# Performance work log

Measured on AMD Instinct MI355X. Metric: run time of the kernel, lower is better.

The kernel has to match this reference:

```python
import jax, jax.numpy as jnp
import numpy as np

B, Q, T, H, W = 8, 100, 50, 256, 256
COST_MASK_W = 1.0  # init kwarg cost_mask
COST_DICE_W = 1.0  # init kwarg cost_dice


def setup_inputs() -> dict:
    key = jax.random.key(0)
    k1, k2 = jax.random.split(key)
    pred_masks = jax.random.normal(k1, (B, Q, H, W), dtype=jnp.float32)
    # binary GT masks (0/1), already at prediction resolution so nearest-interp is identity
    tgt_masks = jax.random.randint(k2, (B, T, H, W), 0, 2).astype(jnp.int32)
    return {"pred_masks": pred_masks, "tgt_masks": tgt_masks}


def reference(pred_masks, tgt_masks):
    # pred_masks: [B, Q, H, W] logits; tgt_masks: [B, T, H, W] binary
    b, q = pred_masks.shape[:2]
    x = pred_masks.reshape(b, q, -1)                      # [B, Q, HW]
    t = tgt_masks.reshape(b, tgt_masks.shape[1], -1).astype(x.dtype)  # [B, T, HW]
    hw = x.shape[-1]

    # batch_sigmoid_ce_loss: BCE-with-logits vs all-ones / all-zeros targets
    pos = jax.nn.softplus(-x)                             # BCE(x, 1)
    neg = jax.nn.softplus(x)                              # BCE(x, 0)
    cost_ce = (jnp.einsum('bqc,btc->bqt', pos, t)
               + jnp.einsum('bqc,btc->bqt', neg, 1.0 - t)) / hw

    # batch_dice_loss
    s = jax.nn.sigmoid(x)
    numerator = 2.0 * jnp.einsum('bqc,btc->bqt', s, t)
    denominator = s.sum(-1)[:, :, None] + t.sum(-1)[:, None, :]
    cost_dice = 1.0 - (numerator + 1.0) / (denominator + 1.0)

    # per-batch cost matrix C [B, Q, T]; the scipy Hungarian step is a
    # host-side CPU call outside the accelerator workload.
    return COST_MASK_W * cost_ce + COST_DICE_W * cost_dice
```

## Files before the change

### kernel.cpp

```cpp
#include <hip/hip_runtime.h>
#include <math.h>

#define B_ 8
#define Q_ 100
#define T_ 50
#define HW_ 65536

#define NSEG 64
#define SEG (HW_ / NSEG)
#define NK32 (SEG / 32)
#define NSTR 52

#define DSZ (B_ * Q_ * NSTR)
#define WS_D1 0
#define WS_D2 DSZ
#define WS_SNEG (2 * DSZ)
#define WS_ST (2 * DSZ + B_ * Q_)
#define WS_TOTAL (2 * DSZ + B_ * Q_ + B_ * T_)

#define PSEG 64
#define SEGP (HW_ / PSEG)
#define NK32P (SEGP / 32)
#define PROWS 101
#define PCOLS 52
#define PTILE ((size_t)PROWS * PCOLS)
#define PBLK ((size_t)B_ * PTILE)
#define D2OFF ((size_t)PSEG * PBLK)
#define WS_NEEDED_BYTES (2ull * D2OFF * 4ull)

typedef __attribute__((ext_vector_type(8))) short bf16x8;
typedef __attribute__((ext_vector_type(4))) float f32x4;

__device__ __forceinline__ unsigned short f2bf(float f) {
    union { float f; unsigned u; } v; v.f = f;
    unsigned r = v.u + 0x7FFF + ((v.u >> 16) & 1);
    return (unsigned short)(r >> 16);
}

__global__ __launch_bounds__(256, 2) void gemm_fused_p(const float* __restrict__ pred,
                                                       const int* __restrict__ tgt,
                                                       float* __restrict__ ws) {
    const int seg = blockIdx.x;
    const int b   = blockIdx.y;
    const int tid = threadIdx.x;
    const int wave = tid >> 6;
    const int lane = tid & 63;
    const int quad = lane >> 4;
    const int l16  = lane & 15;

    const float* xptr[2];
    int aones[2];
#pragma unroll
    for (int mt = 0; mt < 2; ++mt) {
        int m = (wave + mt * 4) * 16 + l16;
        aones[mt] = (m == Q_);
        int mr = m < Q_ ? m : Q_ - 1;
        xptr[mt] = pred + ((size_t)b * Q_ + mr) * HW_ + (size_t)seg * SEGP + quad * 8;
    }
    const int* tptr[4];
    short onesv[4];
#pragma unroll
    for (int nt = 0; nt < 4; ++nt) {
        int n = nt * 16 + l16;
        onesv[nt] = (n == T_) ? (short)0x3F80 : (short)0;
        int nr = n < T_ ? n : T_ - 1;
        tptr[nt] = tgt + ((size_t)b * T_ + nr) * HW_ + (size_t)seg * SEGP + quad * 8;
    }

    f32x4 accx[2][4], accs[2][4];
#pragma unroll
    for (int mt = 0; mt < 2; ++mt)
#pragma unroll
        for (int nt = 0; nt < 4; ++nt) {
            accx[mt][nt] = (f32x4)(0.f);
            accs[mt][nt] = (f32x4)(0.f);
        }
    float sneg[2] = {0.f, 0.f};

    float4 xrb[2][2][2];
    int4   trb[2][4][2];

    auto loadraw = [&](int ch, float4 xr[2][2], int4 tr[4][2]) {
        const int k = ch * 32;
#pragma unroll
        for (int mt = 0; mt < 2; ++mt) {
            xr[mt][0] = *(const float4*)(xptr[mt] + k);
            xr[mt][1] = *(const float4*)(xptr[mt] + k + 4);
        }
#pragma unroll
        for (int nt = 0; nt < 4; ++nt) {
            tr[nt][0] = *(const int4*)(tptr[nt] + k);
            tr[nt][1] = *(const int4*)(tptr[nt] + k + 4);
        }
    };

    auto compute = [&](float4 xr[2][2], int4 tr[4][2]) {
        bf16x8 tf[4];
#pragma unroll
        for (int nt = 0; nt < 4; ++nt)
#pragma unroll
            for (int h = 0; h < 2; ++h)
#pragma unroll
                for (int e = 0; e < 4; ++e) {
                    int v = (&tr[nt][h].x)[e];
                    tf[nt][h * 4 + e] = v ? (short)0x3F80 : onesv[nt];
                }
#pragma unroll
        for (int mt = 0; mt < 2; ++mt) {
            bf16x8 xf, sf;
            float sp = 0.f;
#pragma unroll
            for (int h = 0; h < 2; ++h)
#pragma unroll
                for (int e = 0; e < 4; ++e) {
                    float x = (&xr[mt][h].x)[e];
                    float ax = fabsf(x);
                    float ee = __expf(-ax);
                    float d = 1.f + ee;
                    float r1 = __builtin_amdgcn_rcpf(d);
                    float sg = (x >= 0.f) ? r1 : ee * r1;
                    sp += fmaxf(x, 0.f) + 0.69314718056f * __log2f(d);
                    xf[h * 4 + e] = aones[mt] ? (short)0x3F80 : (short)f2bf(x);
                    sf[h * 4 + e] = aones[mt] ? (short)0x3F80 : (short)f2bf(sg);
                }
            sneg[mt] += sp;
#pragma unroll
            for (int nt = 0; nt < 4; ++nt) {
                accx[mt][nt] = __builtin_amdgcn_mfma_f32_16x16x32_bf16(xf, tf[nt], accx[mt][nt], 0, 0, 0);
                accs[mt][nt] = __builtin_amdgcn_mfma_f32_16x16x32_bf16(sf, tf[nt], accs[mt][nt], 0, 0, 0);
            }
        }
    };

    loadraw(0, xrb[0], trb[0]);
#pragma unroll 2
    for (int ch = 0; ch < NK32P; ++ch) {
        const int cb = ch & 1;
        if (ch + 1 < NK32P) loadraw(ch + 1, xrb[cb ^ 1], trb[cb ^ 1]);
        compute(xrb[cb], trb[cb]);
    }

    float* d1 = ws + (size_t)(seg * B_ + b) * PTILE;
    float* d2 = d1 + D2OFF;

#pragma unroll
    for (int mt = 0; mt < 2; ++mt) {
        float v = sneg[mt];
        v += __shfl_xor(v, 16);
        v += __shfl_xor(v, 32);
        int m = (wave + mt * 4) * 16 + l16;
        if (quad == 0 && m < Q_) d1[(size_t)m * PCOLS + 51] = v;
    }
#pragma unroll
    for (int mt = 0; mt < 2; ++mt) {
        int mtile = (wave + mt * 4) * 16;
#pragma unroll
        for (int nt = 0; nt < 4; ++nt) {
            int n = nt * 16 + l16;
#pragma unroll
            for (int r = 0; r < 4; ++r) {
                int m = mtile + quad * 4 + r;
                if (m <= Q_ && n <= T_) {
                    size_t idx = (size_t)m * PCOLS + n;
                    d1[idx] = accx[mt][nt][r];
                    d2[idx] = accs[mt][nt][r];
                }
            }
        }
    }
}

__global__ void finalize_p(const float* __restrict__ ws, float* __restrict__ out) {
    int i = blockIdx.x * blockDim.x + threadIdx.x;
    if (i >= B_ * Q_ * T_) return;
    int b = i / (Q_ * T_);
    int r = i % (Q_ * T_);
    int q = r / T_;
    int t = r % T_;
    const float* d1 = ws;
    const float* d2 = ws + D2OFF;
    size_t offq = ((size_t)b * PROWS + q) * PCOLS;
    size_t offo = ((size_t)b * PROWS + Q_) * PCOLS;
    float dx = 0.f, ds = 0.f, ss = 0.f, sn = 0.f, stv = 0.f;
#pragma unroll 4
    for (int s = 0; s < PSEG; ++s) {
        size_t base = (size_t)s * PBLK + (size_t)b * PTILE;
        dx  += d1[base + (size_t)q * PCOLS + t];
        ds  += d2[base + (size_t)q * PCOLS + t];
        ss  += d2[base + (size_t)q * PCOLS + T_];
        sn  += d1[base + (size_t)q * PCOLS + 51];
        stv += d1[base + (size_t)Q_ * PCOLS + t];
    }
    (void)offq; (void)offo;
    float ce = (sn - dx) * (1.f / (float)HW_);
    float dice = 1.f - (2.f * ds + 1.f) / (ss + stv + 1.f);
    out[i] = ce + dice;
}

__global__ void zero_ws(float* ws) {
    int i = blockIdx.x * blockDim.x + threadIdx.x;
    if (i < WS_TOTAL) ws[i] = 0.f;
}

__global__ __launch_bounds__(256, 2) void gemm_fused(const float* __restrict__ pred,
                                                     const int* __restrict__ tgt,
                                                     float* __restrict__ ws) {
    const int seg = blockIdx.x;
    const int b   = blockIdx.y;
    const int tid = threadIdx.x;
    const int wave = tid >> 6;
    const int lane = tid & 63;
    const int quad = lane >> 4;
    const int l16  = lane & 15;

    const float* xptr[2];
#pragma unroll
    for (int mt = 0; mt < 2; ++mt) {
        int m = (wave + mt * 4) * 16 + l16;
        int mr = m < Q_ ? m : Q_ - 1;
        xptr[mt] = pred + ((size_t)b * Q_ + mr) * HW_ + (size_t)seg * SEG + quad * 8;
    }
    const int* tptr[4];
    int ones[4];
#pragma unroll
    for (int nt = 0; nt < 4; ++nt) {
        int n = nt * 16 + l16;
        ones[nt] = (n == T_);
        int nr = n < T_ ? n : T_ - 1;
        tptr[nt] = tgt + ((size_t)b * T_ + nr) * HW_ + (size_t)seg * SEG + quad * 8;
    }

    f32x4 accx[2][4], accs[2][4];
#pragma unroll
    for (int mt = 0; mt < 2; ++mt)
#pragma unroll
        for (int nt = 0; nt < 4; ++nt) {
            accx[mt][nt] = (f32x4)(0.f);
            accs[mt][nt] = (f32x4)(0.f);
        }
    float sneg[2] = {0.f, 0.f};
    float stq[4] = {0.f, 0.f, 0.f, 0.f};

    float4 xrb[2][2][2];
    int4   trb[2][4][2];

    auto loadraw = [&](int ch, float4 xr[2][2], int4 tr[4][2]) {
        const int k = ch * 32;
#pragma unroll
        for (int mt = 0; mt < 2; ++mt) {
            xr[mt][0] = *(const float4*)(xptr[mt] + k);
            xr[mt][1] = *(const float4*)(xptr[mt] + k + 4);
        }
#pragma unroll
        for (int nt = 0; nt < 4; ++nt) {
            tr[nt][0] = *(const int4*)(tptr[nt] + k);
            tr[nt][1] = *(const int4*)(tptr[nt] + k + 4);
        }
    };

    auto compute = [&](float4 xr[2][2], int4 tr[4][2]) {
        bf16x8 tf[4];
#pragma unroll
        for (int nt = 0; nt < 4; ++nt) {
            float cnt = 0.f;
#pragma unroll
            for (int h = 0; h < 2; ++h)
#pragma unroll
                for (int e = 0; e < 4; ++e) {
                    int v = (&tr[nt][h].x)[e];
                    tf[nt][h * 4 + e] = (v || ones[nt]) ? (short)0x3F80 : (short)0;
                    cnt += v ? 1.f : 0.f;
                }
            stq[nt] += cnt;
        }
#pragma unroll
        for (int mt = 0; mt < 2; ++mt) {
            bf16x8 xf, sf;
            float sp = 0.f;
#pragma unroll
            for (int h = 0; h < 2; ++h)
#pragma unroll
                for (int e = 0; e < 4; ++e) {
                    float x = (&xr[mt][h].x)[e];
                    float ax = fabsf(x);
                    float ee = __expf(-ax);
                    float d = 1.f + ee;
                    float r1 = __builtin_amdgcn_rcpf(d);
                    float sg = (x >= 0.f) ? r1 : ee * r1;
                    sp += fmaxf(x, 0.f) + 0.69314718056f * __log2f(d);
                    xf[h * 4 + e] = (short)f2bf(x);
                    sf[h * 4 + e] = (short)f2bf(sg);
                }
            sneg[mt] += sp;
#pragma unroll
            for (int nt = 0; nt < 4; ++nt) {
                accx[mt][nt] = __builtin_amdgcn_mfma_f32_16x16x32_bf16(xf, tf[nt], accx[mt][nt], 0, 0, 0);
                accs[mt][nt] = __builtin_amdgcn_mfma_f32_16x16x32_bf16(sf, tf[nt], accs[mt][nt], 0, 0, 0);
            }
        }
    };

    loadraw(0, xrb[0], trb[0]);
#pragma unroll 2
    for (int ch = 0; ch < NK32; ++ch) {
        const int cb = ch & 1;
        if (ch + 1 < NK32) loadraw(ch + 1, xrb[cb ^ 1], trb[cb ^ 1]);
        compute(xrb[cb], trb[cb]);
    }

#pragma unroll
    for (int mt = 0; mt < 2; ++mt) {
        float v = sneg[mt];
        v += __shfl_xor(v, 16);
        v += __shfl_xor(v, 32);
        int m = (wave + mt * 4) * 16 + l16;
        if (quad == 0 && m < Q_) atomicAdd(&ws[WS_SNEG + b * Q_ + m], v);
    }
    if (wave == 0) {
#pragma unroll
        for (int nt = 0; nt < 4; ++nt) {
            float v = stq[nt];
            v += __shfl_xor(v, 16);
            v += __shfl_xor(v, 32);
            int n = nt * 16 + l16;
            if (quad == 0 && n < T_) atomicAdd(&ws[WS_ST + b * T_ + n], v);
        }
    }
#pragma unroll
    for (int mt = 0; mt < 2; ++mt) {
        int mtile = (wave + mt * 4) * 16;
#pragma unroll
        for (int nt = 0; nt < 4; ++nt) {
            int n = nt * 16 + l16;
#pragma unroll
            for (int r = 0; r < 4; ++r) {
                int m = mtile + quad * 4 + r;
                if (m < Q_) {
                    size_t idx = ((size_t)b * Q_ + m) * NSTR + n;
                    if (n < T_) atomicAdd(&ws[WS_D1 + idx], accx[mt][nt][r]);
                    if (n <= T_) atomicAdd(&ws[WS_D2 + idx], accs[mt][nt][r]);
                }
            }
        }
    }
}

__global__ void finalize(const float* __restrict__ ws, float* __restrict__ out) {
    int i = blockIdx.x * blockDim.x + threadIdx.x;
    if (i >= B_ * Q_ * T_) return;
    int b = i / (Q_ * T_);
    int r = i % (Q_ * T_);
    int q = r / T_;
    int t = r % T_;
    float dx   = ws[WS_D1 + ((size_t)b * Q_ + q) * NSTR + t];
    float ds   = ws[WS_D2 + ((size_t)b * Q_ + q) * NSTR + t];
    float ssum = ws[WS_D2 + ((size_t)b * Q_ + q) * NSTR + T_];
    float st   = ws[WS_ST + b * T_ + t];
    float sneg = ws[WS_SNEG + b * Q_ + q];
    float ce = (sneg - dx) * (1.f / (float)HW_);
    float dice = 1.f - (2.f * ds + 1.f) / (ssum + st + 1.f);
    out[i] = ce + dice;
}

extern "C" void kernel_launch(void* const* d_in, const int* in_sizes, int n_in,
                              void* d_out, int out_size, void* d_ws, size_t ws_size,
                              hipStream_t stream) {
    const float* pred = (const float*)d_in[0];
    const int* tgt = (const int*)d_in[1];
    float* ws = (float*)d_ws;
    float* out = (float*)d_out;

    if (ws_size >= WS_NEEDED_BYTES) {
        dim3 g(PSEG, B_, 1);
        gemm_fused_p<<<g, 256, 0, stream>>>(pred, tgt, ws);
        finalize_p<<<(B_ * Q_ * T_ + 255) / 256, 256, 0, stream>>>(ws, out);
    } else {
        zero_ws<<<(WS_TOTAL + 255) / 256, 256, 0, stream>>>(ws);
        dim3 g(NSEG, B_, 1);
        gemm_fused<<<g, 256, 0, stream>>>(pred, tgt, ws);
        finalize<<<(B_ * Q_ * T_ + 255) / 256, 256, 0, stream>>>(ws, out);
    }
}
```

Before: 382.3 us.

## Bit-pack target masks and split-K GEMM with two-stage partial reduction

Adds a pre-pass that uses wave ballots to pack the int32 target masks into bitmasks. The fused MFMA GEMM then reads one 32-bit word per 32 columns instead of 32 int32 values, and expands the bits into bf16 ones and zeros in registers. PSEG doubles to 128 and occupancy is raised. The per-segment partials are reduced in a separate kernel with float4 loads before a slimmer finalize. This cuts target-mask traffic and improves parallelism, at the cost of two extra launches, more partial-sum traffic, and a larger workspace requirement.

```diff
diff --git a/kernel.cpp b/kernel.cpp
--- a/kernel.cpp
+++ b/kernel.cpp
@@ -1,4 +1,5 @@
 #include <hip/hip_runtime.h>
+#include <hip/hip_bf16.h>
 #include <math.h>
 
 #define B_ 8
@@ -18,7 +19,7 @@
 #define WS_ST (2 * DSZ + B_ * Q_)
 #define WS_TOTAL (2 * DSZ + B_ * Q_ + B_ * T_)
 
-#define PSEG 64
+#define PSEG 128
 #define SEGP (HW_ / PSEG)
 #define NK32P (SEGP / 32)
 #define PROWS 101
@@ -28,6 +29,10 @@
 #define D2OFF ((size_t)PSEG * PBLK)
 #define WS_NEEDED_BYTES (2ull * D2OFF * 4ull)
 
+#define BITS_WORDS (B_ * 64 * 2048)
+#define BITS_FOFF (2 * D2OFF)
+#define WS2_NEEDED_BYTES ((2ull * D2OFF + (unsigned long long)BITS_WORDS) * 4ull)
+
 typedef __attribute__((ext_vector_type(8))) short bf16x8;
 typedef __attribute__((ext_vector_type(4))) float f32x4;
 
@@ -35,6 +40,177 @@
     union { float f; unsigned u; } v; v.f = f;
     unsigned r = v.u + 0x7FFF + ((v.u >> 16) & 1);
     return (unsigned short)(r >> 16);
+}
+
+__device__ __forceinline__ unsigned pkbf(float a, float b) {
+    float2 f2; f2.x = a; f2.y = b;
+    __hip_bfloat162 h2 = __float22bfloat162_rn(f2);
+    unsigned u; __builtin_memcpy(&u, &h2, 4); return u;
+}
+
+#define PACK_GROUPS (B_ * 64 * (HW_ / 64))
+__global__ __launch_bounds__(256) void pack_t(const int* __restrict__ tgt,
+                                              unsigned* __restrict__ bits) {
+    int wid = (blockIdx.x * blockDim.x + threadIdx.x) >> 6;
+    int lane = threadIdx.x & 63;
+    int nw = (gridDim.x * blockDim.x) >> 6;
+    for (int g = wid; g < PACK_GROUPS; g += nw) {
+        int b = g >> 16;
+        int row = (g >> 10) & 63;
+        int kbase = (g & 1023) << 6;
+        int v;
+        if (row < T_) v = tgt[((size_t)b * T_ + row) * HW_ + kbase + lane];
+        else v = (row == T_) ? 1 : 0;
+        unsigned long long mask = __ballot(v != 0);
+        size_t widx = ((size_t)(b * 64 + row) << 11) + (kbase >> 5);
+        if (lane == 0) bits[widx] = (unsigned)mask;
+        if (lane == 32) bits[widx + 1] = (unsigned)(mask >> 32);
+    }
+}
+
+__global__ __launch_bounds__(256, 3) void gemm_fused_p2(const float* __restrict__ pred,
+                                                        const unsigned* __restrict__ bits,
+                                                        float* __restrict__ ws) {
+    const int seg = blockIdx.x;
+    const int b   = blockIdx.y;
+    const int tid = threadIdx.x;
+    const int wave = tid >> 6;
+    const int lane = tid & 63;
+    const int quad = lane >> 4;
+    const int l16  = lane & 15;
+
+    const float* xptr[2];
+#pragma unroll
+    for (int mt = 0; mt < 2; ++mt) {
+        int m = (wave + mt * 4) * 16 + l16;
+        int mr = m < Q_ ? m : Q_ - 1;
+        xptr[mt] = pred + ((size_t)b * Q_ + mr) * HW_ + (size_t)seg * SEGP + quad * 8;
+    }
+    const int aones = ((wave + 4) * 16 + l16) == Q_;
+
+    const unsigned* wp[4];
+#pragma unroll
+    for (int nt = 0; nt < 4; ++nt) {
+        int n = nt * 16 + l16;
+        wp[nt] = bits + ((size_t)(b * 64 + n) << 11) + (size_t)seg * NK32P;
+    }
+
+    f32x4 accx[2][4], accs[2][4];
+#pragma unroll
+    for (int mt = 0; mt < 2; ++mt)
+#pragma unroll
+        for (int nt = 0; nt < 4; ++nt) {
+            accx[mt][nt] = (f32x4)(0.f);
+            accs[mt][nt] = (f32x4)(0.f);
+        }
+    float sneg[2] = {0.f, 0.f};
+
+    float4   xrb[2][2][2];
+    unsigned wrb[2][4];
+
+    auto loadraw = [&](int ch, float4 xr[2][2], unsigned wr[4]) {
+#pragma unroll
+        for (int nt = 0; nt < 4; ++nt) wr[nt] = wp[nt][ch];
+        const int k = ch * 32;
+#pragma unroll
+        for (int mt = 0; mt < 2; ++mt) {
+            xr[mt][0] = *(const float4*)(xptr[mt] + k);
+            xr[mt][1] = *(const float4*)(xptr[mt] + k + 4);
+        }
+    };
+
+    auto compute = [&](float4 xr[2][2], unsigned wr[4]) {
+        bf16x8 tf[4];
+#pragma unroll
+        for (int nt = 0; nt < 4; ++nt) {
+            unsigned mw = (wr[nt] >> (quad << 3)) & 0xFFu;
+            unsigned uu[4];
+#pragma unroll
+            for (int j = 0; j < 4; ++j) {
+                uu[j] = ((mw & 1u) * 0x3F80u) | (((mw & 2u) * 0x3F80u) << 15);
+                mw >>= 2;
+            }
+            __builtin_memcpy(&tf[nt], uu, 16);
+        }
+#pragma unroll
+        for (int mt = 0; mt < 2; ++mt) {
+            float xv8[8], sg8[8];
+            float sp = 0.f;
+#pragma unroll
+            for (int h = 0; h < 2; ++h)
+#pragma unroll
+                for (int e = 0; e < 4; ++e) {
+                    int i = h * 4 + e;
+                    float x = (&xr[mt][h].x)[e];
+                    xv8[i] = x;
+                    float ax = fabsf(x);
+                    float ee = __expf(-ax);
+                    float d = 1.f + ee;
+                    float r1 = __builtin_amdgcn_rcpf(d);
+                    sg8[i] = (x >= 0.f) ? r1 : ee * r1;
+                    sp += fmaxf(x, 0.f) + 0.69314718056f * __log2f(d);
+                }
+            sneg[mt] += sp;
+            unsigned xu[4], su[4];
+#pragma unroll
+            for (int j = 0; j < 4; ++j) {
+                xu[j] = pkbf(xv8[2 * j], xv8[2 * j + 1]);
+                su[j] = pkbf(sg8[2 * j], sg8[2 * j + 1]);
+            }
+            if (mt == 1) {
+#pragma unroll
+                for (int j = 0; j < 4; ++j) {
+                    xu[j] = aones ? 0x3F803F80u : xu[j];
+                    su[j] = aones ? 0x3F803F80u : su[j];
+                }
+            }
+            bf16x8 xf, sf;
+            __builtin_memcpy(&xf, xu, 16);
+            __builtin_memcpy(&sf, su, 16);
+#pragma unroll
+            for (int nt = 0; nt < 4; ++nt) {
+                accx[mt][nt] = __builtin_amdgcn_mfma_f32_16x16x32_bf16(xf, tf[nt], accx[mt][nt], 0, 0, 0);
+                accs[mt][nt] = __builtin_amdgcn_mfma_f32_16x16x32_bf16(sf, tf[nt], accs[mt][nt], 0, 0, 0);
+            }
+        }
+    };
+
+    loadraw(0, xrb[0], wrb[0]);
+#pragma unroll 2
+    for (int ch = 0; ch < NK32P; ++ch) {
+        const int cb = ch & 1;
+        if (ch + 1 < NK32P) loadraw(ch + 1, xrb[cb ^ 1], wrb[cb ^ 1]);
+        compute(xrb[cb], wrb[cb]);
+    }
+
+    float* d1 = ws + (size_t)(seg * B_ + b) * PTILE;
+    float* d2 = d1 + D2OFF;
+
+#pragma unroll
+    for (int mt = 0; mt < 2; ++mt) {
+        float v = sneg[mt];
+        v += __shfl_xor(v, 16);
+        v += __shfl_xor(v, 32);
+        int m = (wave + mt * 4) * 16 + l16;
+        if (quad == 0 && m < Q_) d1[(size_t)m * PCOLS + 51] = v;
+    }
+#pragma unroll
+    for (int mt = 0; mt < 2; ++mt) {
+        int mtile = (wave + mt * 4) * 16;
+#pragma unroll
+        for (int nt = 0; nt < 4; ++nt) {
+            int n = nt * 16 + l16;
+#pragma unroll
+            for (int r = 0; r < 4; ++r) {
+                int m = mtile + quad * 4 + r;
+                if (m <= Q_ && n <= T_) {
+                    size_t idx = (size_t)m * PCOLS + n;
+                    d1[idx] = accx[mt][nt][r];
+                    d2[idx] = accs[mt][nt][r];
+                }
+            }
+        }
+    }
 }
 
 __global__ __launch_bounds__(256, 2) void gemm_fused_p(const float* __restrict__ pred,
@@ -170,28 +346,42 @@
     }
 }
 
-__global__ void finalize_p(const float* __restrict__ ws, float* __restrict__ out) {
+__global__ void reduce_p4(float* __restrict__ ws) {
+    int j = blockIdx.x * blockDim.x + threadIdx.x;
+    const int Q4 = (int)(PBLK / 4);
+    if (j >= 2 * Q4) return;
+    int y = blockIdx.y;
+    size_t off = (j < Q4) ? ((size_t)j * 4) : (D2OFF + (size_t)(j - Q4) * 4);
+    const float4* p = (const float4*)(ws + off);
+    int s0 = y * (PSEG / 4);
+    float a0 = 0.f, a1 = 0.f, a2 = 0.f, a3 = 0.f;
+#pragma unroll 4
+    for (int s = s0; s < s0 + PSEG / 4; ++s) {
+        float4 v = p[(size_t)s * (PBLK / 4)];
+        a0 += v.x; a1 += v.y; a2 += v.z; a3 += v.w;
+    }
+    float4 r; r.x = a0; r.y = a1; r.z = a2; r.w = a3;
+    *(float4*)(ws + off + (size_t)s0 * PBLK) = r;
+}
+
+__global__ void finalize_p2(const float* __restrict__ ws, float* __restrict__ out) {
     int i = blockIdx.x * blockDim.x + threadIdx.x;
     if (i >= B_ * Q_ * T_) return;
     int b = i / (Q_ * T_);
     int r = i % (Q_ * T_);
     int q = r / T_;
     int t = r % T_;
-    const float* d1 = ws;
-    const float* d2 = ws + D2OFF;
-    size_t offq = ((size_t)b * PROWS + q) * PCOLS;
-    size_t offo = ((size_t)b * PROWS + Q_) * PCOLS;
     float dx = 0.f, ds = 0.f, ss = 0.f, sn = 0.f, stv = 0.f;
-#pragma unroll 4
-    for (int s = 0; s < PSEG; ++s) {
-        size_t base = (size_t)s * PBLK + (size_t)b * PTILE;
-        dx  += d1[base + (size_t)q * PCOLS + t];
-        ds  += d2[base + (size_t)q * PCOLS + t];
-        ss  += d2[base + (size_t)q * PCOLS + T_];
-        sn  += d1[base + (size_t)q * PCOLS + 51];
-        stv += d1[base + (size_t)Q_ * PCOLS + t];
-    }
-    (void)offq; (void)offo;
+#pragma unroll
+    for (int y = 0; y < 4; ++y) {
+        const float* d1 = ws + (size_t)y * 32 * PBLK + (size_t)b * PTILE;
+        const float* d2 = d1 + D2OFF;
+        dx  += d1[(size_t)q * PCOLS + t];
+        ds  += d2[(size_t)q * PCOLS + t];
+        ss  += d2[(size_t)q * PCOLS + T_];
+        sn  += d1[(size_t)q * PCOLS + 51];
+        stv += d1[(size_t)Q_ * PCOLS + t];
+    }
     float ce = (sn - dx) * (1.f / (float)HW_);
     float dice = 1.f - (2.f * ds + 1.f) / (ss + stv + 1.f);
     out[i] = ce + dice;
@@ -370,10 +560,21 @@
     float* ws = (float*)d_ws;
     float* out = (float*)d_out;
 
-    if (ws_size >= WS_NEEDED_BYTES) {
+    const int Q4 = (int)(PBLK / 4);
+    dim3 rg((2 * Q4 + 255) / 256, 4, 1);
+
+    if (ws_size >= WS2_NEEDED_BYTES) {
+        unsigned* bits = (unsigned*)(ws + BITS_FOFF);
+        pack_t<<<2048, 256, 0, stream>>>(tgt, bits);
+        dim3 g(PSEG, B_, 1);
+        gemm_fused_p2<<<g, 256, 0, stream>>>(pred, bits, ws);
+        reduce_p4<<<rg, 256, 0, stream>>>(ws);
+        finalize_p2<<<(B_ * Q_ * T_ + 255) / 256, 256, 0, stream>>>(ws, out);
+    } else if (ws_size >= WS_NEEDED_BYTES) {
         dim3 g(PSEG, B_, 1);
         gemm_fused_p<<<g, 256, 0, stream>>>(pred, tgt, ws);
-        finalize_p<<<(B_ * Q_ * T_ + 255) / 256, 256, 0, stream>>>(ws, out);
+        reduce_p4<<<rg, 256, 0, stream>>>(ws);
+        finalize_p2<<<(B_ * Q_ * T_ + 255) / 256, 256, 0, stream>>>(ws, out);
     } else {
         zero_ws<<<(WS_TOTAL + 255) / 256, 256, 0, stream>>>(ws);
         dim3 g(NSEG, B_, 1);
```

After: 412.0 us. 1.08x slower.

## Bit-pack targets, stage logits via LDS direct loads, two-stage split-K reduction

Applied to the files above, without the earlier changes.

Adds a pre-pass that packs the int32 target masks into per-row bitmasks, so the GEMM kernel reads 1 bit instead of 4 bytes per target element and expands bits to bf16 in registers. The main kernel doubles the K-split to 128 segments and stages logits into swizzled shared memory with global_load_lds, using explicit waitcnt and sched barriers. It also simplifies the sigmoid/softplus math. The final reduction is split into a partial-sum kernel plus a smaller finalize. This trades an extra packing pass over the targets and two more launches for much less target traffic in the GEMM, and it needs a larger workspace, falling back to the old path if that is not available.

```diff
diff --git a/kernel.cpp b/kernel.cpp
--- a/kernel.cpp
+++ b/kernel.cpp
@@ -1,4 +1,5 @@
 #include <hip/hip_runtime.h>
+#include <hip/hip_bf16.h>
 #include <math.h>
 
 #define B_ 8
@@ -6,11 +7,23 @@
 #define T_ 50
 #define HW_ 65536
 
+#define PSEG 128
+#define SEGK (HW_ / PSEG)
+#define NCH (SEGK / 32)
+#define NSPAN 4
+#define PROWS 101
+#define PCOLS 52
+#define PTILE ((size_t)PROWS * PCOLS)
+#define PBLK ((size_t)B_ * PTILE)
+#define D2OFF ((size_t)PSEG * PBLK)
+#define BITS_WORDS (B_ * 64 * 2048)
+#define BITS_FOFF (2 * D2OFF)
+#define WS2_NEEDED_BYTES ((2ull * D2OFF + (unsigned long long)BITS_WORDS) * 4ull)
+
 #define NSEG 64
 #define SEG (HW_ / NSEG)
 #define NK32 (SEG / 32)
 #define NSTR 52
-
 #define DSZ (B_ * Q_ * NSTR)
 #define WS_D1 0
 #define WS_D2 DSZ
@@ -18,16 +31,6 @@
 #define WS_ST (2 * DSZ + B_ * Q_)
 #define WS_TOTAL (2 * DSZ + B_ * Q_ + B_ * T_)
 
-#define PSEG 64
-#define SEGP (HW_ / PSEG)
-#define NK32P (SEGP / 32)
-#define PROWS 101
-#define PCOLS 52
-#define PTILE ((size_t)PROWS * PCOLS)
-#define PBLK ((size_t)B_ * PTILE)
-#define D2OFF ((size_t)PSEG * PBLK)
-#define WS_NEEDED_BYTES (2ull * D2OFF * 4ull)
-
 typedef __attribute__((ext_vector_type(8))) short bf16x8;
 typedef __attribute__((ext_vector_type(4))) float f32x4;
 
@@ -37,9 +40,41 @@
     return (unsigned short)(r >> 16);
 }
 
-__global__ __launch_bounds__(256, 2) void gemm_fused_p(const float* __restrict__ pred,
-                                                       const int* __restrict__ tgt,
-                                                       float* __restrict__ ws) {
+__device__ __forceinline__ unsigned pkbf(float a, float b) {
+    float2 f2; f2.x = a; f2.y = b;
+    __hip_bfloat162 h2 = __float22bfloat162_rn(f2);
+    unsigned u; __builtin_memcpy(&u, &h2, 4); return u;
+}
+
+__device__ __forceinline__ void gld_lds16(const void* g, void* l) {
+    __builtin_amdgcn_global_load_lds((const __attribute__((address_space(1))) void*)g,
+                                     (__attribute__((address_space(3))) void*)l,
+                                     16, 0, 0);
+}
+
+#define PACK_GROUPS (B_ * 64 * (HW_ / 64))
+__global__ __launch_bounds__(256) void pack_t(const int* __restrict__ tgt,
+                                              unsigned* __restrict__ bits) {
+    int wid = (blockIdx.x * blockDim.x + threadIdx.x) >> 6;
+    int lane = threadIdx.x & 63;
+    int nw = (gridDim.x * blockDim.x) >> 6;
+    for (int g = wid; g < PACK_GROUPS; g += nw) {
+        int b = g >> 16;
+        int row = (g >> 10) & 63;
+        int kbase = (g & 1023) << 6;
+        int v;
+        if (row < T_) v = tgt[((size_t)b * T_ + row) * HW_ + kbase + lane];
+        else v = (row == T_) ? 1 : 0;
+        unsigned long long mask = __ballot(v != 0);
+        size_t widx = ((size_t)(b * 64 + row) << 11) + (kbase >> 5);
+        if (lane == 0) bits[widx] = (unsigned)mask;
+        if (lane == 32) bits[widx + 1] = (unsigned)(mask >> 32);
+    }
+}
+
+__global__ __launch_bounds__(256, 2) void gemm_v7(const float* __restrict__ pred,
+                                                  const unsigned* __restrict__ bits,
+                                                  float* __restrict__ ws) {
     const int seg = blockIdx.x;
     const int b   = blockIdx.y;
     const int tid = threadIdx.x;
@@ -47,24 +82,18 @@
     const int lane = tid & 63;
     const int quad = lane >> 4;
     const int l16  = lane & 15;
-
-    const float* xptr[2];
-    int aones[2];
-#pragma unroll
-    for (int mt = 0; mt < 2; ++mt) {
-        int m = (wave + mt * 4) * 16 + l16;
-        aones[mt] = (m == Q_);
-        int mr = m < Q_ ? m : Q_ - 1;
-        xptr[mt] = pred + ((size_t)b * Q_ + mr) * HW_ + (size_t)seg * SEGP + quad * 8;
-    }
-    const int* tptr[4];
-    short onesv[4];
+    const int half = lane >> 5;
+    const int l31  = lane & 31;
+
+    __shared__ float xs[4][4096];
+
+    const float* pb = pred + (size_t)b * Q_ * HW_ + (size_t)seg * SEGK;
+
+    const unsigned* wp[4];
 #pragma unroll
     for (int nt = 0; nt < 4; ++nt) {
         int n = nt * 16 + l16;
-        onesv[nt] = (n == T_) ? (short)0x3F80 : (short)0;
-        int nr = n < T_ ? n : T_ - 1;
-        tptr[nt] = tgt + ((size_t)b * T_ + nr) * HW_ + (size_t)seg * SEGP + quad * 8;
+        wp[nt] = bits + ((size_t)(b * 64 + n) << 11) + (size_t)seg * NCH;
     }
 
     f32x4 accx[2][4], accs[2][4];
@@ -76,54 +105,70 @@
             accs[mt][nt] = (f32x4)(0.f);
         }
     float sneg[2] = {0.f, 0.f};
-
-    float4 xrb[2][2][2];
-    int4   trb[2][4][2];
-
-    auto loadraw = [&](int ch, float4 xr[2][2], int4 tr[4][2]) {
-        const int k = ch * 32;
+    const int aones = ((wave + 4) * 16 + l16) == Q_;
+
+    unsigned wrb[2][4];
+    auto loadbits = [&](int ch, unsigned wr[4]) {
+#pragma unroll
+        for (int nt = 0; nt < 4; ++nt) wr[nt] = wp[nt][ch];
+    };
+
+    auto stage = [&](int s) {
+#pragma unroll
+        for (int i = 0; i < 16; ++i) {
+            const int rl = 2 * i + half;
+            const int tile = (i < 8) ? wave : (wave + 4);
+            int grow = tile * 16 + (rl & 15);
+            grow = grow < Q_ ? grow : Q_ - 1;
+            const int kf = s * 128 + ((l31 ^ (rl & 7)) << 2);
+            gld_lds16(pb + (size_t)grow * HW_ + kf, &xs[wave][i * 256]);
+        }
+    };
+
+    auto compute = [&](float4 xr[2][2], unsigned wr[4]) {
+        bf16x8 tf[4];
+#pragma unroll
+        for (int nt = 0; nt < 4; ++nt) {
+            unsigned mw = (wr[nt] >> (quad << 3)) & 0xFFu;
+            unsigned uu[4];
+#pragma unroll
+            for (int j = 0; j < 4; ++j) {
+                uu[j] = ((mw & 1u) * 0x3F80u) | (((mw & 2u) * 0x3F80u) << 15);
+                mw >>= 2;
+            }
+            __builtin_memcpy(&tf[nt], uu, 16);
+        }
 #pragma unroll
         for (int mt = 0; mt < 2; ++mt) {
-            xr[mt][0] = *(const float4*)(xptr[mt] + k);
-            xr[mt][1] = *(const float4*)(xptr[mt] + k + 4);
-        }
-#pragma unroll
-        for (int nt = 0; nt < 4; ++nt) {
-            tr[nt][0] = *(const int4*)(tptr[nt] + k);
-            tr[nt][1] = *(const int4*)(tptr[nt] + k + 4);
-        }
-    };
-
-    auto compute = [&](float4 xr[2][2], int4 tr[4][2]) {
-        bf16x8 tf[4];
-#pragma unroll
-        for (int nt = 0; nt < 4; ++nt)
-#pragma unroll
-            for (int h = 0; h < 2; ++h)
-#pragma unroll
-                for (int e = 0; e < 4; ++e) {
-                    int v = (&tr[nt][h].x)[e];
-                    tf[nt][h * 4 + e] = v ? (short)0x3F80 : onesv[nt];
+            float xe[8] = {xr[mt][0].x, xr[mt][0].y, xr[mt][0].z, xr[mt][0].w,
+                           xr[mt][1].x, xr[mt][1].y, xr[mt][1].z, xr[mt][1].w};
+            float sg8[8];
+            float sp = 0.f;
+#pragma unroll
+            for (int e = 0; e < 8; ++e) {
+                float x = xe[e];
+                float ee = __expf(-x);
+                float d = 1.f + ee;
+                sg8[e] = __builtin_amdgcn_rcpf(d);
+                sp += fmaf(0.69314718056f, __log2f(d), x);
+            }
+            sneg[mt] += sp;
+            unsigned xu[4], su[4];
+#pragma unroll
+            for (int j = 0; j < 4; ++j) {
+                xu[j] = pkbf(xe[2 * j], xe[2 * j + 1]);
+                su[j] = pkbf(sg8[2 * j], sg8[2 * j + 1]);
+            }
+            if (mt == 1) {
+#pragma unroll
+                for (int j = 0; j < 4; ++j) {
+                    xu[j] = aones ? 0x3F803F80u : xu[j];
+                    su[j] = aones ? 0x3F803F80u : su[j];
                 }
-#pragma unroll
-        for (int mt = 0; mt < 2; ++mt) {
+            }
             bf16x8 xf, sf;
-            float sp = 0.f;
-#pragma unroll
-            for (int h = 0; h < 2; ++h)
-#pragma unroll
-                for (int e = 0; e < 4; ++e) {
-                    float x = (&xr[mt][h].x)[e];
-                    float ax = fabsf(x);
-                    float ee = __expf(-ax);
-                    float d = 1.f + ee;
-                    float r1 = __builtin_amdgcn_rcpf(d);
-                    float sg = (x >= 0.f) ? r1 : ee * r1;
-                    sp += fmaxf(x, 0.f) + 0.69314718056f * __log2f(d);
-                    xf[h * 4 + e] = aones[mt] ? (short)0x3F80 : (short)f2bf(x);
-                    sf[h * 4 + e] = aones[mt] ? (short)0x3F80 : (short)f2bf(sg);
-                }
-            sneg[mt] += sp;
+            __builtin_memcpy(&xf, xu, 16);
+            __builtin_memcpy(&sf, su, 16);
 #pragma unroll
             for (int nt = 0; nt < 4; ++nt) {
                 accx[mt][nt] = __builtin_amdgcn_mfma_f32_16x16x32_bf16(xf, tf[nt], accx[mt][nt], 0, 0, 0);
@@ -132,12 +177,29 @@
         }
     };
 
-    loadraw(0, xrb[0], trb[0]);
-#pragma unroll 2
-    for (int ch = 0; ch < NK32P; ++ch) {
-        const int cb = ch & 1;
-        if (ch + 1 < NK32P) loadraw(ch + 1, xrb[cb ^ 1], trb[cb ^ 1]);
-        compute(xrb[cb], trb[cb]);
+    stage(0);
+    loadbits(0, wrb[0]);
+
+    for (int s = 0; s < NSPAN; ++s) {
+#pragma unroll
+        for (int c = 0; c < 4; ++c) {
+            const int ch = s * 4 + c;
+            if (c == 0) asm volatile("s_waitcnt vmcnt(0)" ::: "memory");
+            float4 xr[2][2];
+#pragma unroll
+            for (int mt = 0; mt < 2; ++mt)
+#pragma unroll
+                for (int j = 0; j < 2; ++j)
+                    xr[mt][j] = *(const float4*)&xs[wave][(mt * 16 + l16) * 128 +
+                                   (((c * 8 + quad * 2 + j) ^ (l16 & 7)) << 2)];
+            if (ch + 1 < NCH) loadbits(ch + 1, wrb[(ch + 1) & 1]);
+            if (c == 3 && s + 1 < NSPAN) {
+                asm volatile("s_waitcnt lgkmcnt(0)" ::: "memory");
+                __builtin_amdgcn_sched_barrier(0);
+                stage(s + 1);
+            }
+            compute(xr, wrb[ch & 1]);
+        }
     }
 
     float* d1 = ws + (size_t)(seg * B_ + b) * PTILE;
@@ -170,28 +232,42 @@
     }
 }
 
-__global__ void finalize_p(const float* __restrict__ ws, float* __restrict__ out) {
+__global__ void reduce_p4(float* __restrict__ ws) {
+    int j = blockIdx.x * blockDim.x + threadIdx.x;
+    const int Q4 = (int)(PBLK / 4);
+    if (j >= 2 * Q4) return;
+    int y = blockIdx.y;
+    size_t off = (j < Q4) ? ((size_t)j * 4) : (D2OFF + (size_t)(j - Q4) * 4);
+    const float4* p = (const float4*)(ws + off);
+    int s0 = y * (PSEG / 4);
+    float a0 = 0.f, a1 = 0.f, a2 = 0.f, a3 = 0.f;
+#pragma unroll 4
+    for (int s = s0; s < s0 + PSEG / 4; ++s) {
+        float4 v = p[(size_t)s * (PBLK / 4)];
+        a0 += v.x; a1 += v.y; a2 += v.z; a3 += v.w;
+    }
+    float4 r; r.x = a0; r.y = a1; r.z = a2; r.w = a3;
+    *(float4*)(ws + off + (size_t)s0 * PBLK) = r;
+}
+
+__global__ void finalize_p2(const float* __restrict__ ws, float* __restrict__ out) {
     int i = blockIdx.x * blockDim.x + threadIdx.x;
     if (i >= B_ * Q_ * T_) return;
     int b = i / (Q_ * T_);
     int r = i % (Q_ * T_);
     int q = r / T_;
     int t = r % T_;
-    const float* d1 = ws;
-    const float* d2 = ws + D2OFF;
-    size_t offq = ((size_t)b * PROWS + q) * PCOLS;
-    size_t offo = ((size_t)b * PROWS + Q_) * PCOLS;
     float dx = 0.f, ds = 0.f, ss = 0.f, sn = 0.f, stv = 0.f;
-#pragma unroll 4
-    for (int s = 0; s < PSEG; ++s) {
-        size_t base = (size_t)s * PBLK + (size_t)b * PTILE;
-        dx  += d1[base + (size_t)q * PCOLS + t];
-        ds  += d2[base + (size_t)q * PCOLS + t];
-        ss  += d2[base + (size_t)q * PCOLS + T_];
-        sn  += d1[base + (size_t)q * PCOLS + 51];
-        stv += d1[base + (size_t)Q_ * PCOLS + t];
-    }
-    (void)offq; (void)offo;
+#pragma unroll
+    for (int y = 0; y < 4; ++y) {
+        const float* d1 = ws + (size_t)y * 32 * PBLK + (size_t)b * PTILE;
+        const float* d2 = d1 + D2OFF;
+        dx  += d1[(size_t)q * PCOLS + t];
+        ds  += d2[(size_t)q * PCOLS + t];
+        ss  += d2[(size_t)q * PCOLS + T_];
+        sn  += d1[(size_t)q * PCOLS + 51];
+        stv += d1[(size_t)Q_ * PCOLS + t];
+    }
     float ce = (sn - dx) * (1.f / (float)HW_);
     float dice = 1.f - (2.f * ds + 1.f) / (ss + stv + 1.f);
     out[i] = ce + dice;
@@ -370,10 +446,15 @@
     float* ws = (float*)d_ws;
     float* out = (float*)d_out;
 
-    if (ws_size >= WS_NEEDED_BYTES) {
+    if (ws_size >= WS2_NEEDED_BYTES) {
+        unsigned* bits = (unsigned*)(ws + BITS_FOFF);
+        pack_t<<<2048, 256, 0, stream>>>(tgt, bits);
         dim3 g(PSEG, B_, 1);
-        gemm_fused_p<<<g, 256, 0, stream>>>(pred, tgt, ws);
-        finalize_p<<<(B_ * Q_ * T_ + 255) / 256, 256, 0, stream>>>(ws, out);
+        gemm_v7<<<g, 256, 0, stream>>>(pred, bits, ws);
+        const int Q4 = (int)(PBLK / 4);
+        dim3 rg((2 * Q4 + 255) / 256, 4, 1);
+        reduce_p4<<<rg, 256, 0, stream>>>(ws);
+        finalize_p2<<<(B_ * Q_ * T_ + 255) / 256, 256, 0, stream>>>(ws, out);
     } else {
         zero_ws<<<(WS_TOTAL + 255) / 256, 256, 0, stream>>>(ws);
         dim3 g(NSEG, B_, 1);
```

Result: slower. 417.4 us (+9.2%).
